# Performance work log

Measured on AMD Instinct MI355X. Metric: run time of the kernel, lower is better.

Reference implementation:

```python
import jax, jax.numpy as jnp
import numpy as np
import math


def _bandwidth(d):
    # gz = 2*Gamma((d+1)/2)/Gamma(d/2); use lgamma for numerical stability.
    gz = 2.0 * math.exp(math.lgamma(0.5 * (d + 1)) - math.lgamma(0.5 * d))
    return 1.0 / (2.0 * gz * gz)


def _kernel_mean(xa, xb, gamma):
    # mean over the [Na, Nb] RBF kernel matrix, squared distance via matmul identity
    sq = (jnp.sum(xa * xa, axis=1)[:, None]
          + jnp.sum(xb * xb, axis=1)[None, :]
          - 2.0 * (xa @ xb.T))
    sq = jnp.maximum(sq, 0.0)  # guard tiny negatives from the identity
    return jnp.mean(jnp.exp(-gamma * sq))


def setup_inputs() -> dict:
    key = jax.random.key(0)
    k1, k2 = jax.random.split(key)
    x1 = jax.random.normal(k1, (8192, 128), dtype=jnp.float32)
    x2 = jax.random.normal(k2, (8192, 128), dtype=jnp.float32)
    return {"x1": x1, "x2": x2}


def reference(x1, x2):
    g1 = _bandwidth(x1.shape[1])
    g2 = _bandwidth(x2.shape[1])
    m11 = _kernel_mean(x1, x1, g1)
    m22 = _kernel_mean(x2, x2, g2)
    m12 = _kernel_mean(x1, x2, g1)
    return jnp.sqrt(m11 - 2.0 * m12 + m22)
```

## Files before the change

### kernel.cpp

```cpp
#include <hip/hip_runtime.h>
#include <cmath>

#define D 128
#define BM 128
#define BN 64
#define NSEG 12
#define LOG2E 1.4426950408889634

typedef __attribute__((ext_vector_type(8))) _Float16 f16x8;
typedef __attribute__((ext_vector_type(4))) float f32x4;
typedef __attribute__((ext_vector_type(2))) float f32x2;

__global__ __launch_bounds__(256) void prep_kernel(
    const float* __restrict__ x1, const float* __restrict__ x2,
    _Float16* __restrict__ xh, float* __restrict__ El,
    double* __restrict__ acc, float gl, int N) {
    int tid = threadIdx.x;
    if (blockIdx.x == 0 && tid < 64) acc[tid] = 0.0;
    int r = blockIdx.x * 16 + (tid >> 4);
    if (r >= 2 * N) return;
    int l = tid & 15;
    const float* row = (r < N) ? x1 + (size_t)r * D : x2 + (size_t)(r - N) * D;
    float4 v0 = ((const float4*)row)[l * 2];
    float4 v1 = ((const float4*)row)[l * 2 + 1];
    float v[8] = {v0.x, v0.y, v0.z, v0.w, v1.x, v1.y, v1.z, v1.w};
    float p = 0.f;
    _Float16 h8[8];
#pragma unroll
    for (int j = 0; j < 8; ++j) {
        p = fmaf(v[j], v[j], p);
        h8[j] = (_Float16)v[j];
    }
    *(uint4*)(xh + (size_t)r * D + l * 8) = *(uint4*)h8;
#pragma unroll
    for (int off = 8; off; off >>= 1) p += __shfl_down(p, off, 16);
    if (l == 0) El[r] = gl * p;
}

__global__ __launch_bounds__(256, 3) void mmd_mfma_kernel(
    const _Float16* __restrict__ xh, const float* __restrict__ El,
    double* __restrict__ acc, float c2l, int N) {
    __shared__ double red[4];

    int tid = threadIdx.x;
    int lane = tid & 63, wave = tid >> 6;
    int quad = lane >> 4, l16 = lane & 15;
    int wrow = (wave & 1) * 64;
    int wcol = (wave >> 1) * 32;

    int nt2 = 2 * N / BM;
    int half = N / BM;
    int p = blockIdx.x / NSEG;
    int s = blockIdx.x % NSEG;
    int tpp = nt2 + 1;
    int q = tpp / NSEG, r = tpp % NSEG;
    int t0 = s * q + (s < r ? s : r);
    int nt = q + (s < r ? 1 : 0);
    int H = 2 * nt;

    auto BI = [&](int tt) { return tt <= p ? p : nt2 - 1 - p; };
    auto BJ = [&](int tt) { return tt <= p ? tt : tt - p - 1; };

    f16x8 a[4][4];
    float4 ea4[4];
    int curA = -1;
    double dsum = 0.0;

    for (int ht = 0; ht < H; ++ht) {
        int tt = t0 + (ht >> 1), h = ht & 1;
        int bi = BI(tt), bj = BJ(tt);
        int aBase = bi * BM;
        int bcolBase = bj * BM + h * BN;
        float w = (bi == bj) ? 1.0f : 2.0f;
        if ((bi < half) != (bj < half)) w = -2.0f;

        if (aBase != curA) {
            curA = aBase;
#pragma unroll
            for (int u = 0; u < 4; ++u) {
                int ar = aBase + wrow + u * 16 + l16;
#pragma unroll
                for (int j = 0; j < 4; ++j) {
                    int g = (j >> 1) * 8 + (j & 1) * 4 + quad;
                    a[u][j] = *(const f16x8*)(xh + (size_t)ar * D + g * 8);
                }
            }
            int arow0 = aBase + wrow + quad * 4;
#pragma unroll
            for (int ti = 0; ti < 4; ++ti)
                ea4[ti] = *(const float4*)&El[arow0 + ti * 16];
        }

        int bcol0 = bcolBase + wcol + l16;
        float ebv0 = El[bcol0];
        float ebv1 = El[bcol0 + 16];

        f32x4 C[4][2];
#pragma unroll
        for (int ti = 0; ti < 4; ++ti)
#pragma unroll
            for (int tj = 0; tj < 2; ++tj) C[ti][tj] = {0.f, 0.f, 0.f, 0.f};

#pragma unroll
        for (int j = 0; j < 4; ++j) {
            int gb = (j >> 1) * 8 + (j & 1) * 4 + quad;
            f16x8 b[2];
#pragma unroll
            for (int u = 0; u < 2; ++u) {
                int br = bcolBase + wcol + u * 16 + l16;
                b[u] = *(const f16x8*)(xh + (size_t)br * D + gb * 8);
            }
#pragma unroll
            for (int ti = 0; ti < 4; ++ti)
#pragma unroll
                for (int tj = 0; tj < 2; ++tj)
                    C[ti][tj] = __builtin_amdgcn_mfma_f32_16x16x32_f16(
                        a[ti][j], b[tj], C[ti][tj], 0, 0, 0);
        }

        f32x2 cc = {c2l, c2l};
        float lsum = 0.f;
#pragma unroll
        for (int tj = 0; tj < 2; ++tj) {
            f32x2 p2 = {0.f, 0.f};
#pragma unroll
            for (int ti = 0; ti < 4; ++ti) {
                f32x4 d = C[ti][tj];
                f32x2 a01 = cc * f32x2{d.x, d.y} + f32x2{ea4[ti].x, ea4[ti].y};
                f32x2 a23 = cc * f32x2{d.z, d.w} + f32x2{ea4[ti].z, ea4[ti].w};
                f32x2 e, e2;
                e.x = __builtin_amdgcn_exp2f(a01.x);
                e.y = __builtin_amdgcn_exp2f(a01.y);
                e2.x = __builtin_amdgcn_exp2f(a23.x);
                e2.y = __builtin_amdgcn_exp2f(a23.y);
                p2 += e + e2;
            }
            lsum = fmaf(p2.x + p2.y,
                        __builtin_amdgcn_exp2f(tj ? ebv1 : ebv0), lsum);
        }
        dsum += (double)lsum * (double)w;
    }

#pragma unroll
    for (int off = 32; off; off >>= 1) dsum += __shfl_down(dsum, off);
    if (lane == 0) red[wave] = dsum;
    __syncthreads();
    if (tid == 0)
        atomicAdd(&acc[blockIdx.x & 63], red[0] + red[1] + red[2] + red[3]);
}

__global__ __launch_bounds__(64) void mmd_finalize_kernel(
    const double* __restrict__ acc, float* __restrict__ out, int N) {
    int l = threadIdx.x;
    double v = acc[l];
#pragma unroll
    for (int off = 32; off; off >>= 1) v += __shfl_down(v, off);
    if (l == 0) {
        double nn = (double)N * (double)N;
        double s = v / nn;
        out[0] = (float)sqrt(s > 0.0 ? s : 0.0);
    }
}

extern "C" void kernel_launch(void* const* d_in, const int* in_sizes, int n_in,
                              void* d_out, int out_size, void* d_ws, size_t ws_size,
                              hipStream_t stream) {
    const float* x1 = (const float*)d_in[0];
    const float* x2 = (const float*)d_in[1];
    int N = in_sizes[0] / D;

    double* acc = (double*)d_ws;
    float* El = (float*)((char*)d_ws + 8192);
    _Float16* xh = (_Float16*)((char*)d_ws + 73728);

    double lg = lgamma(0.5 * (D + 1)) - lgamma(0.5 * D);
    double gz = 2.0 * exp(lg);
    double gamma = 1.0 / (2.0 * gz * gz);
    float gl = (float)(-gamma * LOG2E);
    float c2l = (float)(2.0 * gamma * LOG2E);

    prep_kernel<<<(2 * N + 15) / 16, 256, 0, stream>>>(x1, x2, xh, El, acc, gl, N);

    int nblocks = 64 * NSEG;
    mmd_mfma_kernel<<<nblocks, 256, 0, stream>>>(xh, El, acc, c2l, N);

    mmd_finalize_kernel<<<1, 64, 0, stream>>>(acc, (float*)d_out, N);
}
```

Measured before the change: 131.0 us.

## Double-buffer B fragments in registers and reorganize tile/wave column split

Loads of each sub-tile's B operand fragments now go into two register buffers, and the next sub-tile's B is prefetched while the current one runs its MFMAs and exp epilogue. The aim is to hide global load latency. Each wave now covers a 64-wide column band split into two 32-column sub-steps instead of a 32-column slice of two 64-wide halves. Segments per pair drop from 12 to 8 and the occupancy hint goes from 3 to 2 blocks per CU to make room for the extra registers, which lowers parallelism and latency hiding across waves.

Measured after the change: 131.8 us. No clear change (+0.6%).

```diff
diff --git a/kernel.cpp b/kernel.cpp
--- a/kernel.cpp
+++ b/kernel.cpp
@@ -3,8 +3,7 @@
 
 #define D 128
 #define BM 128
-#define BN 64
-#define NSEG 12
+#define NSEG 8
 #define LOG2E 1.4426950408889634
 
 typedef __attribute__((ext_vector_type(8))) _Float16 f16x8;
@@ -37,7 +36,7 @@
     if (l == 0) El[r] = gl * p;
 }
 
-__global__ __launch_bounds__(256, 3) void mmd_mfma_kernel(
+__global__ __launch_bounds__(256, 2) void mmd_mfma_kernel(
     const _Float16* __restrict__ xh, const float* __restrict__ El,
     double* __restrict__ acc, float c2l, int N) {
     __shared__ double red[4];
@@ -46,7 +45,7 @@
     int lane = tid & 63, wave = tid >> 6;
     int quad = lane >> 4, l16 = lane & 15;
     int wrow = (wave & 1) * 64;
-    int wcol = (wave >> 1) * 32;
+    int wcolBase = (wave >> 1) * 64;
 
     int nt2 = 2 * N / BM;
     int half = N / BM;
@@ -56,24 +55,37 @@
     int q = tpp / NSEG, r = tpp % NSEG;
     int t0 = s * q + (s < r ? s : r);
     int nt = q + (s < r ? 1 : 0);
-    int H = 2 * nt;
+    int S = 2 * nt;
 
     auto BI = [&](int tt) { return tt <= p ? p : nt2 - 1 - p; };
     auto BJ = [&](int tt) { return tt <= p ? tt : tt - p - 1; };
+    auto subCol = [&](int k) {
+        int tt = t0 + (k >> 1);
+        return BJ(tt) * BM + wcolBase + (k & 1) * 32;
+    };
 
     f16x8 a[4][4];
     float4 ea4[4];
     int curA = -1;
     double dsum = 0.0;
-
-    for (int ht = 0; ht < H; ++ht) {
-        int tt = t0 + (ht >> 1), h = ht & 1;
+    f32x2 cc = {c2l, c2l};
+
+    auto loadB = [&](f16x8 (&B)[2][4], int cb) {
+#pragma unroll
+        for (int u = 0; u < 2; ++u) {
+#pragma unroll
+            for (int j = 0; j < 4; ++j) {
+                int g = (j >> 1) * 8 + (j & 1) * 4 + quad;
+                int br = cb + u * 16 + l16;
+                B[u][j] = *(const f16x8*)(xh + (size_t)br * D + g * 8);
+            }
+        }
+    };
+
+    auto computeEpi = [&](const f16x8 (&B)[2][4], int k) {
+        int tt = t0 + (k >> 1);
         int bi = BI(tt), bj = BJ(tt);
         int aBase = bi * BM;
-        int bcolBase = bj * BM + h * BN;
-        float w = (bi == bj) ? 1.0f : 2.0f;
-        if ((bi < half) != (bj < half)) w = -2.0f;
-
         if (aBase != curA) {
             curA = aBase;
 #pragma unroll
@@ -90,35 +102,32 @@
             for (int ti = 0; ti < 4; ++ti)
                 ea4[ti] = *(const float4*)&El[arow0 + ti * 16];
         }
-
-        int bcol0 = bcolBase + wcol + l16;
-        float ebv0 = El[bcol0];
-        float ebv1 = El[bcol0 + 16];
-
+        float w = (bi == bj) ? 1.0f : 2.0f;
+        if ((bi < half) != (bj < half)) w = -2.0f;
+        int cb = bj * BM + wcolBase + (k & 1) * 32;
+        int bcol0 = cb + l16;
+        float eb0 = El[bcol0];
+        float eb1 = El[bcol0 + 16];
+
+        const f32x4 CZ = {0.f, 0.f, 0.f, 0.f};
         f32x4 C[4][2];
 #pragma unroll
-        for (int ti = 0; ti < 4; ++ti)
-#pragma unroll
-            for (int tj = 0; tj < 2; ++tj) C[ti][tj] = {0.f, 0.f, 0.f, 0.f};
-
-#pragma unroll
-        for (int j = 0; j < 4; ++j) {
-            int gb = (j >> 1) * 8 + (j & 1) * 4 + quad;
-            f16x8 b[2];
-#pragma unroll
-            for (int u = 0; u < 2; ++u) {
-                int br = bcolBase + wcol + u * 16 + l16;
-                b[u] = *(const f16x8*)(xh + (size_t)br * D + gb * 8);
-            }
-#pragma unroll
-            for (int ti = 0; ti < 4; ++ti)
-#pragma unroll
-                for (int tj = 0; tj < 2; ++tj)
-                    C[ti][tj] = __builtin_amdgcn_mfma_f32_16x16x32_f16(
-                        a[ti][j], b[tj], C[ti][tj], 0, 0, 0);
-        }
-
-        f32x2 cc = {c2l, c2l};
+        for (int ti = 0; ti < 4; ++ti) {
+            C[ti][0] = __builtin_amdgcn_mfma_f32_16x16x32_f16(
+                a[ti][0], B[0][0], CZ, 0, 0, 0);
+            C[ti][1] = __builtin_amdgcn_mfma_f32_16x16x32_f16(
+                a[ti][0], B[1][0], CZ, 0, 0, 0);
+        }
+#pragma unroll
+        for (int j = 1; j < 4; ++j)
+#pragma unroll
+            for (int ti = 0; ti < 4; ++ti) {
+                C[ti][0] = __builtin_amdgcn_mfma_f32_16x16x32_f16(
+                    a[ti][j], B[0][j], C[ti][0], 0, 0, 0);
+                C[ti][1] = __builtin_amdgcn_mfma_f32_16x16x32_f16(
+                    a[ti][j], B[1][j], C[ti][1], 0, 0, 0);
+            }
+
         float lsum = 0.f;
 #pragma unroll
         for (int tj = 0; tj < 2; ++tj) {
@@ -136,9 +145,18 @@
                 p2 += e + e2;
             }
             lsum = fmaf(p2.x + p2.y,
-                        __builtin_amdgcn_exp2f(tj ? ebv1 : ebv0), lsum);
+                        __builtin_amdgcn_exp2f(tj ? eb1 : eb0), lsum);
         }
         dsum += (double)lsum * (double)w;
+    };
+
+    f16x8 Ba[2][4], Bb[2][4];
+    loadB(Ba, subCol(0));
+    for (int k = 0; k < S; k += 2) {
+        loadB(Bb, subCol(k + 1));
+        computeEpi(Ba, k);
+        loadB(Ba, subCol(k + 2 < S ? k + 2 : 0));
+        computeEpi(Bb, k + 1);
     }
 
 #pragma unroll
```

## Stage B tiles into LDS with async global_load_lds double buffering

Applied to the files above, without the earlier changes.

B-operand rows now go into a per-wave LDS double buffer through global_load_lds with an XOR swizzle, while the next 16-column slice is prefetched during compute. Each wave works on 16-column steps (four per tile) instead of two 32-column halves, and MFMA issue is raised in priority. The aim is to hide global-load latency for B behind the MFMA and exp work, and to avoid bank conflicts on the LDS reads. In exchange it adds 32KB of LDS per block, which may limit occupancy under launch_bounds(256,3), and relies on hand-written vmcnt waits being correct.

After: 109.5 us. 1.2x faster.

```diff
diff --git a/kernel.cpp b/kernel.cpp
--- a/kernel.cpp
+++ b/kernel.cpp
@@ -3,13 +3,18 @@
 
 #define D 128
 #define BM 128
-#define BN 64
 #define NSEG 12
 #define LOG2E 1.4426950408889634
 
 typedef __attribute__((ext_vector_type(8))) _Float16 f16x8;
 typedef __attribute__((ext_vector_type(4))) float f32x4;
 typedef __attribute__((ext_vector_type(2))) float f32x2;
+
+__device__ __forceinline__ void async_cp16(const void* g, void* l) {
+    __builtin_amdgcn_global_load_lds(
+        (__attribute__((address_space(1))) void*)g,
+        (__attribute__((address_space(3))) void*)l, 16, 0, 0);
+}
 
 __global__ __launch_bounds__(256) void prep_kernel(
     const float* __restrict__ x1, const float* __restrict__ x2,
@@ -40,13 +45,13 @@
 __global__ __launch_bounds__(256, 3) void mmd_mfma_kernel(
     const _Float16* __restrict__ xh, const float* __restrict__ El,
     double* __restrict__ acc, float c2l, int N) {
-    __shared__ double red[4];
+    __shared__ float4 smem[4][2][256];
 
     int tid = threadIdx.x;
     int lane = tid & 63, wave = tid >> 6;
     int quad = lane >> 4, l16 = lane & 15;
     int wrow = (wave & 1) * 64;
-    int wcol = (wave >> 1) * 32;
+    int wcolG = (wave >> 1) * 64;
 
     int nt2 = 2 * N / BM;
     int half = N / BM;
@@ -56,23 +61,56 @@
     int q = tpp / NSEG, r = tpp % NSEG;
     int t0 = s * q + (s < r ? s : r);
     int nt = q + (s < r ? 1 : 0);
-    int H = 2 * nt;
-
+    int S = 4 * nt;
+
+    int goff[4];
+#pragma unroll
+    for (int i = 0; i < 4; ++i) {
+        int slot = i * 64 + lane;
+        int rr = slot >> 4;
+        int g = (slot & 15) ^ (rr & 7);
+        goff[i] = rr * D + g * 8;
+    }
+
+    auto stage = [&](int c0, int buf) {
+        const _Float16* src = xh + (size_t)c0 * D;
+#pragma unroll
+        for (int i = 0; i < 4; ++i)
+            async_cp16(src + goff[i], &smem[wave][buf][i * 64 + lane]);
+    };
     auto BI = [&](int tt) { return tt <= p ? p : nt2 - 1 - p; };
     auto BJ = [&](int tt) { return tt <= p ? tt : tt - p - 1; };
+    auto colOf = [&](int k) {
+        int tt = t0 + (k >> 2);
+        return BJ(tt) * BM + wcolG + (k & 3) * 16;
+    };
+
+    stage(colOf(0), 0);
+    stage(colOf(1), 1);
 
     f16x8 a[4][4];
     float4 ea4[4];
     int curA = -1;
     double dsum = 0.0;
-
-    for (int ht = 0; ht < H; ++ht) {
-        int tt = t0 + (ht >> 1), h = ht & 1;
+    f32x2 cc = {c2l, c2l};
+
+    for (int k = 0; k < S; ++k) {
+        int tt = t0 + (k >> 2);
         int bi = BI(tt), bj = BJ(tt);
         int aBase = bi * BM;
-        int bcolBase = bj * BM + h * BN;
         float w = (bi == bj) ? 1.0f : 2.0f;
         if ((bi < half) != (bj < half)) w = -2.0f;
+        int buf = k & 1;
+        int c0 = bj * BM + wcolG + (k & 3) * 16;
+
+        if (k + 1 < S) {
+            asm volatile("s_waitcnt vmcnt(4)" ::: "memory");
+        } else {
+            asm volatile("s_waitcnt vmcnt(0)" ::: "memory");
+        }
+        __builtin_amdgcn_sched_barrier(0);
+
+        float eb = El[c0 + l16];
 
         if (aBase != curA) {
             curA = aBase;
@@ -91,58 +129,51 @@
                 ea4[ti] = *(const float4*)&El[arow0 + ti * 16];
         }
 
-        int bcol0 = bcolBase + wcol + l16;
-        float ebv0 = El[bcol0];
-        float ebv1 = El[bcol0 + 16];
-
-        f32x4 C[4][2];
-#pragma unroll
-        for (int ti = 0; ti < 4; ++ti)
-#pragma unroll
-            for (int tj = 0; tj < 2; ++tj) C[ti][tj] = {0.f, 0.f, 0.f, 0.f};
-
+        f16x8 b[4];
 #pragma unroll
         for (int j = 0; j < 4; ++j) {
-            int gb = (j >> 1) * 8 + (j & 1) * 4 + quad;
-            f16x8 b[2];
-#pragma unroll
-            for (int u = 0; u < 2; ++u) {
-                int br = bcolBase + wcol + u * 16 + l16;
-                b[u] = *(const f16x8*)(xh + (size_t)br * D + gb * 8);
-            }
+            int kc = (j >> 1) * 8 + (j & 1) * 4 + quad;
+            b[j] = *(const f16x8*)&smem[wave][buf][l16 * 16 + (kc ^ (l16 & 7))];
+        }
+        asm volatile("s_waitcnt lgkmcnt(0)" ::: "memory");
+        __builtin_amdgcn_sched_barrier(0);
+        if (k + 2 < S) stage(colOf(k + 2), buf);
+        __builtin_amdgcn_sched_barrier(0);
+
+        f32x4 C[4];
+#pragma unroll
+        for (int ti = 0; ti < 4; ++ti) C[ti] = {0.f, 0.f, 0.f, 0.f};
+
+        __builtin_amdgcn_s_setprio(1);
+#pragma unroll
+        for (int j = 0; j < 4; ++j)
 #pragma unroll
             for (int ti = 0; ti < 4; ++ti)
-#pragma unroll
-                for (int tj = 0; tj < 2; ++tj)
-                    C[ti][tj] = __builtin_amdgcn_mfma_f32_16x16x32_f16(
-                        a[ti][j], b[tj], C[ti][tj], 0, 0, 0);
-        }
-
-        f32x2 cc = {c2l, c2l};
-        float lsum = 0.f;
-#pragma unroll
-        for (int tj = 0; tj < 2; ++tj) {
-            f32x2 p2 = {0.f, 0.f};
-#pragma unroll
-            for (int ti = 0; ti < 4; ++ti) {
-                f32x4 d = C[ti][tj];
-                f32x2 a01 = cc * f32x2{d.x, d.y} + f32x2{ea4[ti].x, ea4[ti].y};
-                f32x2 a23 = cc * f32x2{d.z, d.w} + f32x2{ea4[ti].z, ea4[ti].w};
-                f32x2 e, e2;
-                e.x = __builtin_amdgcn_exp2f(a01.x);
-                e.y = __builtin_amdgcn_exp2f(a01.y);
-                e2.x = __builtin_amdgcn_exp2f(a23.x);
-                e2.y = __builtin_amdgcn_exp2f(a23.y);
-                p2 += e + e2;
-            }
-            lsum = fmaf(p2.x + p2.y,
-                        __builtin_amdgcn_exp2f(tj ? ebv1 : ebv0), lsum);
-        }
+                C[ti] = __builtin_amdgcn_mfma_f32_16x16x32_f16(
+                    a[ti][j], b[j], C[ti], 0, 0, 0);
+        __builtin_amdgcn_s_setprio(0);
+
+        f32x2 p2 = {0.f, 0.f};
+#pragma unroll
+        for (int ti = 0; ti < 4; ++ti) {
+            f32x4 d = C[ti];
+            f32x2 a01 = cc * f32x2{d.x, d.y} + f32x2{ea4[ti].x, ea4[ti].y};
+            f32x2 a23 = cc * f32x2{d.z, d.w} + f32x2{ea4[ti].z, ea4[ti].w};
+            f32x2 e, e2;
+            e.x = __builtin_amdgcn_exp2f(a01.x);
+            e.y = __builtin_amdgcn_exp2f(a01.y);
+            e2.x = __builtin_amdgcn_exp2f(a23.x);
+            e2.y = __builtin_amdgcn_exp2f(a23.y);
+            p2 += e + e2;
+        }
+        float lsum = (p2.x + p2.y) * __builtin_amdgcn_exp2f(eb);
         dsum += (double)lsum * (double)w;
     }
 
 #pragma unroll
     for (int off = 32; off; off >>= 1) dsum += __shfl_down(dsum, off);
+    __syncthreads();
+    double* red = (double*)&smem[0][0][0];
     if (lane == 0) red[wave] = dsum;
     __syncthreads();
     if (tid == 0)
```
